# Performance work log

Measured on AMD Instinct MI355X. Metric: run time of the kernel, lower is better.

The kernel has to match this reference:

```python
import jax, jax.numpy as jnp
import numpy as np

M, N, C, D = 2, 8, 1024, 256  # n_routers, num_adapters, channel_dim, down_sample_size
B, S = 32, 512


def setup_inputs() -> dict:
    key = jax.random.key(0)
    k1, k2, k3, k4, k5 = jax.random.split(key, 5)
    x = jax.random.normal(k1, (B, S, C), dtype=jnp.float32)
    expert_index = jax.random.randint(k2, (M, B), 0, N, dtype=jnp.int32)
    down_w = jax.random.normal(k3, (M, N, C, D), dtype=jnp.float32) * 0.01
    down_b = jax.random.normal(k4, (M, N, D), dtype=jnp.float32) * 0.01
    up_w = jax.random.normal(k5, (M, N, D, C), dtype=jnp.float32) * 0.01
    return {"x": x, "expert_index": expert_index, "down_w": down_w,
            "down_b": down_b, "up_w": up_w}


def reference(x, expert_index, down_w, down_b, up_w):
    # Gather per-(router, batch-element) adapter weights along the adapter axis.
    idx = expert_index  # [M, B]
    bw_down = jnp.take_along_axis(down_w, idx[:, :, None, None], axis=1)  # [M, B, C, D]
    bb_down = jnp.take_along_axis(down_b, idx[:, :, None], axis=1)        # [M, B, D]
    bw_up = jnp.take_along_axis(up_w, idx[:, :, None, None], axis=1)      # [M, B, D, C]
    # z = swish(x @ W_down + b_down)  -> [M, B, S, D]
    z = jnp.einsum('bsc,mbcd->mbsd', x, bw_down) + bb_down[:, :, None, :]
    z = jax.nn.silu(z)
    # u = z @ W_up -> [M, B, S, C]
    u = jnp.einsum('mbsd,mbdc->mbsc', z, bw_up)
    return u
```

## Files before the change

kernel.cpp:

```cpp
#include <hip/hip_runtime.h>
#include <stdint.h>

typedef unsigned short u16;
typedef __bf16 bf16x8 __attribute__((ext_vector_type(8)));
typedef float f32x4 __attribute__((ext_vector_type(4)));

#define MM 2
#define NN 8
#define CC 1024
#define DD 256
#define BB 32
#define SS 512

__device__ __forceinline__ u16 f2bf(float f) {
  uint32_t u = __float_as_uint(f);
  u += 0x7FFFu + ((u >> 16) & 1u);
  return (u16)(u >> 16);
}

__device__ __forceinline__ uint32_t pack2(float a, float b) {
  return (uint32_t)f2bf(a) | ((uint32_t)f2bf(b) << 16);
}

__device__ __forceinline__ void async16(const void* g, void* l) {
  __builtin_amdgcn_global_load_lds(
      (const __attribute__((address_space(1))) uint32_t*)g,
      (__attribute__((address_space(3))) uint32_t*)l, 16, 0, 0);
}

__global__ __launch_bounds__(256) void prep_w(
    const float* __restrict__ dw, u16* __restrict__ wdT,
    const float* __restrict__ uw, u16* __restrict__ wuT) {
  __shared__ float tile[64][33];
  int bid = blockIdx.x;
  const float* src; u16* dst; int K, N, tk, tn;
  if (bid < 2048) {
    K = CC; N = DD;
    const int slab = bid >> 7, t = bid & 127;
    tk = t >> 3; tn = t & 7;
    src = dw + (size_t)slab * K * N;
    dst = wdT + (size_t)slab * K * N;
  } else {
    bid -= 2048;
    K = DD; N = CC;
    const int slab = bid >> 7, t = bid & 127;
    tk = t >> 5; tn = t & 31;
    src = uw + (size_t)slab * K * N;
    dst = wuT + (size_t)slab * K * N;
  }
  const int k0 = tk * 64, n0 = tn * 32;
  const int tx = threadIdx.x & 31, ty = threadIdx.x >> 5;
#pragma unroll
  for (int i = 0; i < 64; i += 8)
    tile[ty + i][tx] = src[(size_t)(k0 + ty + i) * N + n0 + tx];
  __syncthreads();
  uint32_t* dst32 = reinterpret_cast<uint32_t*>(dst);
#pragma unroll
  for (int i = 0; i < 32; i += 8) {
    const int nr = ty + i;
    dst32[((size_t)(n0 + nr) * K + k0) / 2 + tx] =
        pack2(tile[2 * tx][nr], tile[2 * tx + 1][nr]);
  }
}

__global__ __launch_bounds__(512, 2) void fused_adapter(
    const float* __restrict__ x, const u16* __restrict__ wdT,
    const u16* __restrict__ wuT, const float* __restrict__ db,
    const int* __restrict__ eidx, float* __restrict__ out) {
  __shared__ __align__(16) u16 smA[2][128 * 32];
  __shared__ __align__(16) u16 smB[3][256 * 32];
  __shared__ __align__(16) u16 zl[8 * 128 * 32];

  const int pair = blockIdx.y;
  const int m = pair >> 5;
  const int b = pair & 31;
  const int e = eidx[pair];
  const int s0 = blockIdx.x * 128;

  const int tid = threadIdx.x;
  const int lane = tid & 63;
  const int wave = tid >> 6;
  const int quad = lane >> 4;
  const int l16 = lane & 15;
  const int fx = (l16 >> 1) & 3;

  const int wr = (wave >> 2) * 64;
  const int wc = (wave & 3) * 64;

  const u16* Bd = wdT + (size_t)(m * NN + e) * DD * CC;
  const u16* Bu = wuT + (size_t)(m * NN + e) * CC * DD;

  const float* bias_p = db + (size_t)(m * NN + e) * DD;
  float biasr[4];
#pragma unroll
  for (int j = 0; j < 4; ++j) biasr[j] = bias_p[wc + j * 16 + l16];

  const int arow = tid >> 2;
  const int achk = tid & 3;
  const float* gAx = x + ((size_t)b * SS + s0 + arow) * CC + achk * 8;
  const int lAoff = arow * 32 + ((achk ^ ((arow >> 1) & 3)) * 8);

  const int srow = lane >> 2;
  const int qx = (lane & 3) ^ ((srow >> 1) & 3);
  const u16* gBd = Bd + (size_t)(wave * 32 + srow) * CC + qx * 8;
  const u16* gBu = Bu + (size_t)(wave * 32 + srow) * DD + qx * 8;
  const int lB0o = wave * 32 * 32;
  const int lB1o = lB0o + 16 * 32;

  f32x4 acc[4][4];
#pragma unroll
  for (int i = 0; i < 4; ++i)
#pragma unroll
    for (int j = 0; j < 4; ++j) acc[i][j] = (f32x4){0.f, 0.f, 0.f, 0.f};

  {
    float4 a0 = *reinterpret_cast<const float4*>(gAx);
    float4 a1 = *reinterpret_cast<const float4*>(gAx + 4);
    async16(gBd, &smB[0][lB0o]);
    async16(gBd + 16 * CC, &smB[0][lB1o]);
    async16(gBd + 32, &smB[1][lB0o]);
    async16(gBd + 16 * CC + 32, &smB[1][lB1o]);
    *reinterpret_cast<uint4*>(&smA[0][lAoff]) =
        make_uint4(pack2(a0.x, a0.y), pack2(a0.z, a0.w),
                   pack2(a1.x, a1.y), pack2(a1.z, a1.w));
  }
  asm volatile("s_waitcnt vmcnt(2) lgkmcnt(0)" ::: "memory");
  __builtin_amdgcn_s_barrier();

  for (int kk = 0; kk < 32; ++kk) {
    const int slot = kk % 3, nslot = (kk + 2) % 3;
    const int abuf = kk & 1;
    float4 nA0, nA1;
    if (kk < 31) {
      const int ko = (kk + 1) * 32;
      nA0 = *reinterpret_cast<const float4*>(gAx + ko);
      nA1 = *reinterpret_cast<const float4*>(gAx + ko + 4);
    }
    if (kk < 30) {
      const int ko2 = (kk + 2) * 32;
      async16(gBd + ko2, &smB[nslot][lB0o]);
      async16(gBd + 16 * CC + ko2, &smB[nslot][lB1o]);
    } else {
      const int g = kk - 30;
      async16(gBu + g * 32, &smB[nslot][lB0o]);
      async16(gBu + 16 * DD + g * 32, &smB[nslot][lB1o]);
    }
    bf16x8 af[4], bfr[4];
#pragma unroll
    for (int i = 0; i < 4; ++i)
      af[i] = *reinterpret_cast<const bf16x8*>(
          &smA[abuf][(wr + i * 16 + l16) * 32 + (quad ^ fx) * 8]);
#pragma unroll
    for (int j = 0; j < 4; ++j)
      bfr[j] = *reinterpret_cast<const bf16x8*>(
          &smB[slot][(wc + j * 16 + l16) * 32 + (quad ^ fx) * 8]);
#pragma unroll
    for (int i = 0; i < 4; ++i)
#pragma unroll
      for (int j = 0; j < 4; ++j)
        acc[i][j] = __builtin_amdgcn_mfma_f32_16x16x32_bf16(af[i], bfr[j], acc[i][j], 0, 0, 0);
    if (kk < 31) {
      *reinterpret_cast<uint4*>(&smA[abuf ^ 1][lAoff]) =
          make_uint4(pack2(nA0.x, nA0.y), pack2(nA0.z, nA0.w),
                     pack2(nA1.x, nA1.y), pack2(nA1.z, nA1.w));
    }
    asm volatile("s_waitcnt vmcnt(2) lgkmcnt(0)" ::: "memory");
    __builtin_amdgcn_s_barrier();
  }

#pragma unroll
  for (int j = 0; j < 4; ++j) {
    const int d = wc + j * 16 + l16;
    const int kt = d >> 5;
    const int kl = d & 31;
    const int slot0 = kl >> 3;
    const int kin = kl & 7;
#pragma unroll
    for (int i = 0; i < 4; ++i) {
      const int zr = wr + i * 16 + quad * 4;
#pragma unroll
      for (int r = 0; r < 4; ++r) {
        const int row = zr + r;
        float v = acc[i][j][r] + biasr[j];
        v = v / (1.f + __expf(-v));
        zl[kt * 4096 + row * 32 + ((slot0 ^ ((row >> 1) & 3)) * 8) + kin] = f2bf(v);
      }
    }
  }
  asm volatile("s_waitcnt vmcnt(2) lgkmcnt(0)" ::: "memory");
  __builtin_amdgcn_s_barrier();

  float* ob = out + ((size_t)pair * SS + s0) * CC;

  for (int g = 0; g < 32; ++g) {
    const int slot = (g + 2) % 3, nslot = (g + 1) % 3;
    const int ct = g >> 3;
    const int it = g & 7;
    if (g < 30) {
      const int g2 = g + 2;
      const size_t ro = (size_t)(g2 >> 3) * 256 * DD + (g2 & 7) * 32;
      async16(gBu + ro, &smB[nslot][lB0o]);
      async16(gBu + ro + 16 * DD, &smB[nslot][lB1o]);
    }
    if (it == 0) {
#pragma unroll
      for (int i = 0; i < 4; ++i)
#pragma unroll
        for (int j = 0; j < 4; ++j) acc[i][j] = (f32x4){0.f, 0.f, 0.f, 0.f};
    }
    bf16x8 af[4], bfr[4];
#pragma unroll
    for (int i = 0; i < 4; ++i)
      af[i] = *reinterpret_cast<const bf16x8*>(
          &zl[it * 4096 + (wr + i * 16 + l16) * 32 + (quad ^ fx) * 8]);
#pragma unroll
    for (int j = 0; j < 4; ++j)
      bfr[j] = *reinterpret_cast<const bf16x8*>(
          &smB[slot][(wc + j * 16 + l16) * 32 + (quad ^ fx) * 8]);
#pragma unroll
    for (int i = 0; i < 4; ++i)
#pragma unroll
      for (int j = 0; j < 4; ++j)
        acc[i][j] = __builtin_amdgcn_mfma_f32_16x16x32_bf16(af[i], bfr[j], acc[i][j], 0, 0, 0);
    if (it == 7) {
#pragma unroll
      for (int j = 0; j < 4; ++j) {
        const int c = ct * 256 + wc + j * 16 + l16;
#pragma unroll
        for (int i = 0; i < 4; ++i) {
          const int sr = wr + i * 16 + quad * 4;
#pragma unroll
          for (int r = 0; r < 4; ++r)
            ob[(size_t)(sr + r) * CC + c] = acc[i][j][r];
        }
      }
    }
    if (g < 31) {
      if (g == 30)
        asm volatile("s_waitcnt vmcnt(0) lgkmcnt(0)" ::: "memory");
      else if (it == 7)
        asm volatile("s_waitcnt vmcnt(18) lgkmcnt(0)" ::: "memory");
      else
        asm volatile("s_waitcnt vmcnt(2) lgkmcnt(0)" ::: "memory");
      __builtin_amdgcn_s_barrier();
    }
  }
}

extern "C" void kernel_launch(void* const* d_in, const int* in_sizes, int n_in,
                              void* d_out, int out_size, void* d_ws, size_t ws_size,
                              hipStream_t stream) {
  const float* x  = (const float*)d_in[0];
  const int* eidx = (const int*)d_in[1];
  const float* dw = (const float*)d_in[2];
  const float* db = (const float*)d_in[3];
  const float* uw = (const float*)d_in[4];
  float* out = (float*)d_out;

  char* ws = (char*)d_ws;
  u16* wdT = (u16*)(ws);
  u16* wuT = (u16*)(ws + (size_t)8 * 1024 * 1024);

  prep_w<<<dim3(4096), dim3(256), 0, stream>>>(dw, wdT, uw, wuT);
  fused_adapter<<<dim3(SS / 128, MM * BB), dim3(512), 0, stream>>>(
      x, wdT, wuT, db, eidx, out);
}
```

Before: 268.8 us.

## Deepen activation prefetch, raise MFMA priority, and relax epilogue waits

In the first GEMM, the fp32 activation tile is now prefetched two k-steps ahead into alternating register sets, and the loop is unrolled by 2. This is meant to hide global load latency better, and the k-loop wait is loosened to vmcnt(4) to match. MFMA blocks in both GEMMs are wrapped in s_setprio so they get issue priority, and the modulo-3 slot arithmetic is replaced by rotating counters. In the second GEMM the wait around output-store iterations becomes vmcnt(63). Because vmcnt also counts stores on this architecture, that wait may no longer guarantee the next B tile has arrived, which risks a correctness problem.

```diff
diff --git a/kernel.cpp b/kernel.cpp
--- a/kernel.cpp
+++ b/kernel.cpp
@@ -26,6 +26,12 @@
   __builtin_amdgcn_global_load_lds(
       (const __attribute__((address_space(1))) uint32_t*)g,
       (__attribute__((address_space(3))) uint32_t*)l, 16, 0, 0);
+}
+
+__device__ __forceinline__ void packA(const float4& a, const float4& b, u16* dst) {
+  *reinterpret_cast<uint4*>(dst) =
+      make_uint4(pack2(a.x, a.y), pack2(a.z, a.w),
+                 pack2(b.x, b.y), pack2(b.z, b.w));
 }
 
 __global__ __launch_bounds__(256) void prep_w(
@@ -113,6 +119,8 @@
 #pragma unroll
     for (int j = 0; j < 4; ++j) acc[i][j] = (f32x4){0.f, 0.f, 0.f, 0.f};
 
+  float4 rA0a, rA0b, rA1a, rA1b;
+
   {
     float4 a0 = *reinterpret_cast<const float4*>(gAx);
     float4 a1 = *reinterpret_cast<const float4*>(gAx + 4);
@@ -120,51 +128,61 @@
     async16(gBd + 16 * CC, &smB[0][lB1o]);
     async16(gBd + 32, &smB[1][lB0o]);
     async16(gBd + 16 * CC + 32, &smB[1][lB1o]);
-    *reinterpret_cast<uint4*>(&smA[0][lAoff]) =
-        make_uint4(pack2(a0.x, a0.y), pack2(a0.z, a0.w),
-                   pack2(a1.x, a1.y), pack2(a1.z, a1.w));
+    rA1a = *reinterpret_cast<const float4*>(gAx + 32);
+    rA1b = *reinterpret_cast<const float4*>(gAx + 36);
+    packA(a0, a1, &smA[0][lAoff]);
   }
   asm volatile("s_waitcnt vmcnt(2) lgkmcnt(0)" ::: "memory");
   __builtin_amdgcn_s_barrier();
 
+  int slot_c = 0;
+#pragma unroll 2
   for (int kk = 0; kk < 32; ++kk) {
-    const int slot = kk % 3, nslot = (kk + 2) % 3;
-    const int abuf = kk & 1;
-    float4 nA0, nA1;
-    if (kk < 31) {
-      const int ko = (kk + 1) * 32;
-      nA0 = *reinterpret_cast<const float4*>(gAx + ko);
-      nA1 = *reinterpret_cast<const float4*>(gAx + ko + 4);
-    }
+    const int slot = slot_c;
+    const int nslot = slot >= 1 ? slot - 1 : 2;
+    slot_c = slot < 2 ? slot + 1 : 0;
+
     if (kk < 30) {
-      const int ko2 = (kk + 2) * 32;
-      async16(gBd + ko2, &smB[nslot][lB0o]);
-      async16(gBd + 16 * CC + ko2, &smB[nslot][lB1o]);
+      const int ko = (kk + 2) * 32;
+      if ((kk & 1) == 0) {
+        rA0a = *reinterpret_cast<const float4*>(gAx + ko);
+        rA0b = *reinterpret_cast<const float4*>(gAx + ko + 4);
+      } else {
+        rA1a = *reinterpret_cast<const float4*>(gAx + ko);
+        rA1b = *reinterpret_cast<const float4*>(gAx + ko + 4);
+      }
+      async16(gBd + ko, &smB[nslot][lB0o]);
+      async16(gBd + 16 * CC + ko, &smB[nslot][lB1o]);
     } else {
-      const int g = kk - 30;
-      async16(gBu + g * 32, &smB[nslot][lB0o]);
-      async16(gBu + 16 * DD + g * 32, &smB[nslot][lB1o]);
-    }
+      const int gg = kk - 30;
+      async16(gBu + gg * 32, &smB[nslot][lB0o]);
+      async16(gBu + 16 * DD + gg * 32, &smB[nslot][lB1o]);
+    }
+
     bf16x8 af[4], bfr[4];
 #pragma unroll
     for (int i = 0; i < 4; ++i)
       af[i] = *reinterpret_cast<const bf16x8*>(
-          &smA[abuf][(wr + i * 16 + l16) * 32 + (quad ^ fx) * 8]);
+          &smA[kk & 1][(wr + i * 16 + l16) * 32 + (quad ^ fx) * 8]);
 #pragma unroll
     for (int j = 0; j < 4; ++j)
       bfr[j] = *reinterpret_cast<const bf16x8*>(
           &smB[slot][(wc + j * 16 + l16) * 32 + (quad ^ fx) * 8]);
+    __builtin_amdgcn_s_setprio(1);
 #pragma unroll
     for (int i = 0; i < 4; ++i)
 #pragma unroll
       for (int j = 0; j < 4; ++j)
         acc[i][j] = __builtin_amdgcn_mfma_f32_16x16x32_bf16(af[i], bfr[j], acc[i][j], 0, 0, 0);
+    __builtin_amdgcn_s_setprio(0);
+
     if (kk < 31) {
-      *reinterpret_cast<uint4*>(&smA[abuf ^ 1][lAoff]) =
-          make_uint4(pack2(nA0.x, nA0.y), pack2(nA0.z, nA0.w),
-                     pack2(nA1.x, nA1.y), pack2(nA1.z, nA1.w));
-    }
-    asm volatile("s_waitcnt vmcnt(2) lgkmcnt(0)" ::: "memory");
+      if ((kk & 1) == 0) packA(rA1a, rA1b, &smA[1][lAoff]);
+      else               packA(rA0a, rA0b, &smA[0][lAoff]);
+    }
+
+    if (kk < 30) asm volatile("s_waitcnt vmcnt(4) lgkmcnt(0)" ::: "memory");
+    else         asm volatile("s_waitcnt vmcnt(2) lgkmcnt(0)" ::: "memory");
     __builtin_amdgcn_s_barrier();
   }
 
@@ -192,8 +210,11 @@
 
   float* ob = out + ((size_t)pair * SS + s0) * CC;
 
+  int slot2_c = 2;
   for (int g = 0; g < 32; ++g) {
-    const int slot = (g + 2) % 3, nslot = (g + 1) % 3;
+    const int slot = slot2_c;
+    const int nslot = slot >= 1 ? slot - 1 : 2;
+    slot2_c = slot < 2 ? slot + 1 : 0;
     const int ct = g >> 3;
     const int it = g & 7;
     if (g < 30) {
@@ -217,12 +238,15 @@
     for (int j = 0; j < 4; ++j)
       bfr[j] = *reinterpret_cast<const bf16x8*>(
           &smB[slot][(wc + j * 16 + l16) * 32 + (quad ^ fx) * 8]);
+    __builtin_amdgcn_s_setprio(1);
 #pragma unroll
     for (int i = 0; i < 4; ++i)
 #pragma unroll
       for (int j = 0; j < 4; ++j)
         acc[i][j] = __builtin_amdgcn_mfma_f32_16x16x32_bf16(af[i], bfr[j], acc[i][j], 0, 0, 0);
+    __builtin_amdgcn_s_setprio(0);
     if (it == 7) {
+      asm volatile("" ::: "memory");
 #pragma unroll
       for (int j = 0; j < 4; ++j) {
         const int c = ct * 256 + wc + j * 16 + l16;
@@ -238,8 +262,8 @@
     if (g < 31) {
       if (g == 30)
         asm volatile("s_waitcnt vmcnt(0) lgkmcnt(0)" ::: "memory");
-      else if (it == 7)
-        asm volatile("s_waitcnt vmcnt(18) lgkmcnt(0)" ::: "memory");
+      else if (it == 7 || it == 0)
+        asm volatile("s_waitcnt vmcnt(63) lgkmcnt(0)" ::: "memory");
       else
         asm volatile("s_waitcnt vmcnt(2) lgkmcnt(0)" ::: "memory");
       __builtin_amdgcn_s_barrier();
```

Measured after the change: 271.1 us. No clear change (+0.9%).

## Double K-tile depth to 64 with double-buffered pipeline and MFMA priority

Applied to the files above, without the earlier changes.

Widens each pipeline step from 32 to 64 along the reduction dimension in both GEMM phases, halving the number of barriers. Replaces the three-slot B ring with two buffers and a new 8-chunk XOR swizzle, and raises wave priority around MFMA bursts. The trade-off is shallower prefetch with full vmcnt(0) waits, which also wait on outstanding output stores, plus larger LDS use.

```diff
diff --git a/kernel.cpp b/kernel.cpp
--- a/kernel.cpp
+++ b/kernel.cpp
@@ -67,8 +67,8 @@
     const float* __restrict__ x, const u16* __restrict__ wdT,
     const u16* __restrict__ wuT, const float* __restrict__ db,
     const int* __restrict__ eidx, float* __restrict__ out) {
-  __shared__ __align__(16) u16 smA[2][128 * 32];
-  __shared__ __align__(16) u16 smB[3][256 * 32];
+  __shared__ __align__(16) u16 smA[2][128 * 64];
+  __shared__ __align__(16) u16 smB[2][256 * 64];
   __shared__ __align__(16) u16 zl[8 * 128 * 32];
 
   const int pair = blockIdx.y;
@@ -83,6 +83,7 @@
   const int quad = lane >> 4;
   const int l16 = lane & 15;
   const int fx = (l16 >> 1) & 3;
+  const int fxr = l16 & 7;
 
   const int wr = (wave >> 2) * 64;
   const int wc = (wave & 3) * 64;
@@ -96,16 +97,13 @@
   for (int j = 0; j < 4; ++j) biasr[j] = bias_p[wc + j * 16 + l16];
 
   const int arow = tid >> 2;
-  const int achk = tid & 3;
-  const float* gAx = x + ((size_t)b * SS + s0 + arow) * CC + achk * 8;
-  const int lAoff = arow * 32 + ((achk ^ ((arow >> 1) & 3)) * 8);
-
-  const int srow = lane >> 2;
-  const int qx = (lane & 3) ^ ((srow >> 1) & 3);
-  const u16* gBd = Bd + (size_t)(wave * 32 + srow) * CC + qx * 8;
-  const u16* gBu = Bu + (size_t)(wave * 32 + srow) * DD + qx * 8;
-  const int lB0o = wave * 32 * 32;
-  const int lB1o = lB0o + 16 * 32;
+  const int c0 = tid & 3;
+  const float* gAx = x + ((size_t)b * SS + s0 + arow) * CC;
+  const int lA0 = arow * 64 + ((c0 ^ (arow & 7)) * 8);
+  const int lA1 = arow * 64 + (((c0 + 4) ^ (arow & 7)) * 8);
+
+  const int r_l = lane >> 3;
+  const int sx = (lane & 7) ^ r_l;
 
   f32x4 acc[4][4];
 #pragma unroll
@@ -114,57 +112,72 @@
     for (int j = 0; j < 4; ++j) acc[i][j] = (f32x4){0.f, 0.f, 0.f, 0.f};
 
   {
-    float4 a0 = *reinterpret_cast<const float4*>(gAx);
-    float4 a1 = *reinterpret_cast<const float4*>(gAx + 4);
-    async16(gBd, &smB[0][lB0o]);
-    async16(gBd + 16 * CC, &smB[0][lB1o]);
-    async16(gBd + 32, &smB[1][lB0o]);
-    async16(gBd + 16 * CC + 32, &smB[1][lB1o]);
-    *reinterpret_cast<uint4*>(&smA[0][lAoff]) =
+    float4 a0 = *reinterpret_cast<const float4*>(gAx + c0 * 8);
+    float4 a1 = *reinterpret_cast<const float4*>(gAx + c0 * 8 + 4);
+    float4 a2 = *reinterpret_cast<const float4*>(gAx + (c0 + 4) * 8);
+    float4 a3 = *reinterpret_cast<const float4*>(gAx + (c0 + 4) * 8 + 4);
+#pragma unroll
+    for (int s = 0; s < 4; ++s)
+      async16(Bd + (size_t)(wave * 32 + s * 8 + r_l) * CC + sx * 8,
+              &smB[0][(wave * 32 + s * 8) * 64]);
+    *reinterpret_cast<uint4*>(&smA[0][lA0]) =
         make_uint4(pack2(a0.x, a0.y), pack2(a0.z, a0.w),
                    pack2(a1.x, a1.y), pack2(a1.z, a1.w));
-  }
-  asm volatile("s_waitcnt vmcnt(2) lgkmcnt(0)" ::: "memory");
+    *reinterpret_cast<uint4*>(&smA[0][lA1]) =
+        make_uint4(pack2(a2.x, a2.y), pack2(a2.z, a2.w),
+                   pack2(a3.x, a3.y), pack2(a3.z, a3.w));
+  }
+  asm volatile("s_waitcnt vmcnt(0) lgkmcnt(0)" ::: "memory");
   __builtin_amdgcn_s_barrier();
 
-  for (int kk = 0; kk < 32; ++kk) {
-    const int slot = kk % 3, nslot = (kk + 2) % 3;
-    const int abuf = kk & 1;
-    float4 nA0, nA1;
-    if (kk < 31) {
-      const int ko = (kk + 1) * 32;
-      nA0 = *reinterpret_cast<const float4*>(gAx + ko);
-      nA1 = *reinterpret_cast<const float4*>(gAx + ko + 4);
-    }
-    if (kk < 30) {
-      const int ko2 = (kk + 2) * 32;
-      async16(gBd + ko2, &smB[nslot][lB0o]);
-      async16(gBd + 16 * CC + ko2, &smB[nslot][lB1o]);
+  for (int kk = 0; kk < 16; ++kk) {
+    const int cur = kk & 1, nxt = cur ^ 1;
+    float4 a0, a1, a2, a3;
+    if (kk < 15) {
+      const float* gA = gAx + (kk + 1) * 64;
+      a0 = *reinterpret_cast<const float4*>(gA + c0 * 8);
+      a1 = *reinterpret_cast<const float4*>(gA + c0 * 8 + 4);
+      a2 = *reinterpret_cast<const float4*>(gA + (c0 + 4) * 8);
+      a3 = *reinterpret_cast<const float4*>(gA + (c0 + 4) * 8 + 4);
+      const int ko = (kk + 1) * 64;
+#pragma unroll
+      for (int s = 0; s < 4; ++s)
+        async16(Bd + (size_t)(wave * 32 + s * 8 + r_l) * CC + ko + sx * 8,
+                &smB[nxt][(wave * 32 + s * 8) * 64]);
     } else {
-      const int g = kk - 30;
-      async16(gBu + g * 32, &smB[nslot][lB0o]);
-      async16(gBu + 16 * DD + g * 32, &smB[nslot][lB1o]);
-    }
-    bf16x8 af[4], bfr[4];
-#pragma unroll
-    for (int i = 0; i < 4; ++i)
-      af[i] = *reinterpret_cast<const bf16x8*>(
-          &smA[abuf][(wr + i * 16 + l16) * 32 + (quad ^ fx) * 8]);
-#pragma unroll
-    for (int j = 0; j < 4; ++j)
-      bfr[j] = *reinterpret_cast<const bf16x8*>(
-          &smB[slot][(wc + j * 16 + l16) * 32 + (quad ^ fx) * 8]);
-#pragma unroll
-    for (int i = 0; i < 4; ++i)
+#pragma unroll
+      for (int s = 0; s < 4; ++s)
+        async16(Bu + (size_t)(wave * 32 + s * 8 + r_l) * DD + sx * 8,
+                &smB[nxt][(wave * 32 + s * 8) * 64]);
+    }
+#pragma unroll
+    for (int h = 0; h < 2; ++h) {
+      bf16x8 af[4], bfr[4];
+#pragma unroll
+      for (int i = 0; i < 4; ++i)
+        af[i] = *reinterpret_cast<const bf16x8*>(
+            &smA[cur][(wr + i * 16 + l16) * 64 + ((h * 4 + quad) ^ fxr) * 8]);
 #pragma unroll
       for (int j = 0; j < 4; ++j)
-        acc[i][j] = __builtin_amdgcn_mfma_f32_16x16x32_bf16(af[i], bfr[j], acc[i][j], 0, 0, 0);
-    if (kk < 31) {
-      *reinterpret_cast<uint4*>(&smA[abuf ^ 1][lAoff]) =
-          make_uint4(pack2(nA0.x, nA0.y), pack2(nA0.z, nA0.w),
-                     pack2(nA1.x, nA1.y), pack2(nA1.z, nA1.w));
-    }
-    asm volatile("s_waitcnt vmcnt(2) lgkmcnt(0)" ::: "memory");
+        bfr[j] = *reinterpret_cast<const bf16x8*>(
+            &smB[cur][(wc + j * 16 + l16) * 64 + ((h * 4 + quad) ^ fxr) * 8]);
+      __builtin_amdgcn_s_setprio(1);
+#pragma unroll
+      for (int i = 0; i < 4; ++i)
+#pragma unroll
+        for (int j = 0; j < 4; ++j)
+          acc[i][j] = __builtin_amdgcn_mfma_f32_16x16x32_bf16(af[i], bfr[j], acc[i][j], 0, 0, 0);
+      __builtin_amdgcn_s_setprio(0);
+    }
+    if (kk < 15) {
+      *reinterpret_cast<uint4*>(&smA[nxt][lA0]) =
+          make_uint4(pack2(a0.x, a0.y), pack2(a0.z, a0.w),
+                     pack2(a1.x, a1.y), pack2(a1.z, a1.w));
+      *reinterpret_cast<uint4*>(&smA[nxt][lA1]) =
+          make_uint4(pack2(a2.x, a2.y), pack2(a2.z, a2.w),
+                     pack2(a3.x, a3.y), pack2(a3.z, a3.w));
+    }
+    asm volatile("s_waitcnt vmcnt(0) lgkmcnt(0)" ::: "memory");
     __builtin_amdgcn_s_barrier();
   }
 
@@ -187,42 +200,49 @@
       }
     }
   }
-  asm volatile("s_waitcnt vmcnt(2) lgkmcnt(0)" ::: "memory");
+  asm volatile("s_waitcnt lgkmcnt(0)" ::: "memory");
   __builtin_amdgcn_s_barrier();
 
   float* ob = out + ((size_t)pair * SS + s0) * CC;
 
-  for (int g = 0; g < 32; ++g) {
-    const int slot = (g + 2) % 3, nslot = (g + 1) % 3;
-    const int ct = g >> 3;
-    const int it = g & 7;
-    if (g < 30) {
-      const int g2 = g + 2;
-      const size_t ro = (size_t)(g2 >> 3) * 256 * DD + (g2 & 7) * 32;
-      async16(gBu + ro, &smB[nslot][lB0o]);
-      async16(gBu + ro + 16 * DD, &smB[nslot][lB1o]);
-    }
-    if (it == 0) {
+  for (int g = 0; g < 16; ++g) {
+    const int cur2 = g & 1, nxt2 = cur2 ^ 1;
+    const int ct = g >> 2;
+    const int it2 = g & 3;
+    if (g < 15) {
+      const int g2 = g + 1;
+      const size_t ro = (size_t)(g2 >> 2) * 256 * DD + (g2 & 3) * 64;
+#pragma unroll
+      for (int s = 0; s < 4; ++s)
+        async16(Bu + ro + (size_t)(wave * 32 + s * 8 + r_l) * DD + sx * 8,
+                &smB[nxt2][(wave * 32 + s * 8) * 64]);
+    }
+    if (it2 == 0) {
 #pragma unroll
       for (int i = 0; i < 4; ++i)
 #pragma unroll
         for (int j = 0; j < 4; ++j) acc[i][j] = (f32x4){0.f, 0.f, 0.f, 0.f};
     }
-    bf16x8 af[4], bfr[4];
-#pragma unroll
-    for (int i = 0; i < 4; ++i)
-      af[i] = *reinterpret_cast<const bf16x8*>(
-          &zl[it * 4096 + (wr + i * 16 + l16) * 32 + (quad ^ fx) * 8]);
-#pragma unroll
-    for (int j = 0; j < 4; ++j)
-      bfr[j] = *reinterpret_cast<const bf16x8*>(
-          &smB[slot][(wc + j * 16 + l16) * 32 + (quad ^ fx) * 8]);
-#pragma unroll
-    for (int i = 0; i < 4; ++i)
+#pragma unroll
+    for (int h = 0; h < 2; ++h) {
+      bf16x8 af[4], bfr[4];
+#pragma unroll
+      for (int i = 0; i < 4; ++i)
+        af[i] = *reinterpret_cast<const bf16x8*>(
+            &zl[(it2 * 2 + h) * 4096 + (wr + i * 16 + l16) * 32 + (quad ^ fx) * 8]);
 #pragma unroll
       for (int j = 0; j < 4; ++j)
-        acc[i][j] = __builtin_amdgcn_mfma_f32_16x16x32_bf16(af[i], bfr[j], acc[i][j], 0, 0, 0);
-    if (it == 7) {
+        bfr[j] = *reinterpret_cast<const bf16x8*>(
+            &smB[cur2][(wc + j * 16 + l16) * 64 + ((h * 4 + quad) ^ fxr) * 8]);
+      __builtin_amdgcn_s_setprio(1);
+#pragma unroll
+      for (int i = 0; i < 4; ++i)
+#pragma unroll
+        for (int j = 0; j < 4; ++j)
+          acc[i][j] = __builtin_amdgcn_mfma_f32_16x16x32_bf16(af[i], bfr[j], acc[i][j], 0, 0, 0);
+      __builtin_amdgcn_s_setprio(0);
+    }
+    if (it2 == 3) {
 #pragma unroll
       for (int j = 0; j < 4; ++j) {
         const int c = ct * 256 + wc + j * 16 + l16;
@@ -235,13 +255,8 @@
         }
       }
     }
-    if (g < 31) {
-      if (g == 30)
-        asm volatile("s_waitcnt vmcnt(0) lgkmcnt(0)" ::: "memory");
-      else if (it == 7)
-        asm volatile("s_waitcnt vmcnt(18) lgkmcnt(0)" ::: "memory");
-      else
-        asm volatile("s_waitcnt vmcnt(2) lgkmcnt(0)" ::: "memory");
+    if (g < 15) {
+      asm volatile("s_waitcnt vmcnt(0) lgkmcnt(0)" ::: "memory");
       __builtin_amdgcn_s_barrier();
     }
   }
```

New measurement: 247.3 us. 1.09x faster.
